# Kernel tuning notes

Measured on AMD Instinct MI355X. Metric: run time of the kernel, lower is better.

## Reference

```python
import jax, jax.numpy as jnp
import numpy as np


def _conv1x1(x, w, b):
    # x: [B,C,H,W], w: [O,C], b: [O] -> [B,O,H,W]
    return jnp.einsum('bchw,oc->bohw', x, w) + b[None, :, None, None]


def _maxpool2x2(x):
    # MaxPool2d(kernel_size=2, stride=2), VALID padding
    return jax.lax.reduce_window(
        x, -jnp.inf, jax.lax.max,
        window_dimensions=(1, 1, 2, 2),
        window_strides=(1, 1, 2, 2),
        padding='VALID')


def setup_inputs() -> dict:
    key = jax.random.key(0)
    ks = jax.random.split(key, 9)
    B, C, H, W = 8, 256, 64, 64
    c = 128  # in_channels // channel_scale_factor
    s = 0.05
    return {
        'x': jax.random.normal(ks[0], (B, C, H, W), jnp.float32),
        'theta_w': jax.random.normal(ks[1], (c, C), jnp.float32) * s,
        'theta_b': jax.random.normal(ks[2], (c,), jnp.float32) * s,
        'phi_w': jax.random.normal(ks[3], (c, C), jnp.float32) * s,
        'phi_b': jax.random.normal(ks[4], (c,), jnp.float32) * s,
        'g_w': jax.random.normal(ks[5], (c, C), jnp.float32) * s,
        'g_b': jax.random.normal(ks[6], (c,), jnp.float32) * s,
        'wz_w': jax.random.normal(ks[7], (C, c), jnp.float32) * s,
        'wz_b': jax.random.normal(ks[8], (C,), jnp.float32) * s,
    }


def reference(x, theta_w, theta_b, phi_w, phi_b, g_w, g_b, wz_w, wz_b):
    B, C, H, W = x.shape
    c = theta_w.shape[0]
    ox = x
    theta = _conv1x1(x, theta_w, theta_b)              # [B,c,H,W]
    xp = _maxpool2x2(x)                                # [B,C,h,w]
    phi = _conv1x1(xp, phi_w, phi_b)                   # [B,c,h,w]
    gi = _conv1x1(xp, g_w, g_b)                        # [B,c,h,w]

    N = H * W
    M = phi.shape[2] * phi.shape[3]
    theta1 = theta.reshape(B, c, N).transpose(0, 2, 1)  # [B,N,c]
    phi1 = phi.reshape(B, c, M)                         # [B,c,M]
    gi1 = gi.reshape(B, c, M).transpose(0, 2, 1)        # [B,M,c]

    m1 = jnp.einsum('bnc,bcm->bnm', theta1, phi1)       # [B,N,M] attention scores
    m1 = jax.nn.softmax(m1, axis=2)
    m2 = jnp.einsum('bnm,bmc->bnc', m1, gi1)            # [B,N,c]
    # Faithful to torch .view: raw-buffer reinterpretation, no transpose
    m3 = m2.reshape(B, c, H, W)
    m4 = _conv1x1(m3, wz_w, wz_b)                       # [B,C,H,W]
    return m4 + ox
```

## Files before the change

### kernel.cpp

```cpp
#include <hip/hip_runtime.h>
#include <math.h>

#define BATCH 8
#define CINCH 256
#define CMID  128
#define NPIX  4096
#define MPIX  1024

typedef __attribute__((ext_vector_type(8))) short bf16x8;
typedef __attribute__((ext_vector_type(4))) short s16x4;
typedef __attribute__((ext_vector_type(4))) float f32x4;

static __device__ __forceinline__ short f2bf(float f) {
    unsigned u = __float_as_uint(f);
    u = (u + 0x7fffu + ((u >> 16) & 1u)) >> 16;
    return (short)u;
}
static __device__ __forceinline__ float bf2f(short s) {
    return __uint_as_float(((unsigned)(unsigned short)s) << 16);
}

static __device__ __forceinline__ void gl16(const void* g, void* l) {
    __builtin_amdgcn_global_load_lds(
        (const __attribute__((address_space(1))) void*)g,
        (__attribute__((address_space(3))) void*)l, 16, 0, 0);
}

__global__ __launch_bounds__(256)
void wcvt_k(const float* __restrict__ a, const float* __restrict__ b,
            const float* __restrict__ c, const float* __restrict__ d,
            short* __restrict__ o)
{
    int i = (blockIdx.x * 256 + threadIdx.x) * 4;
    if (i < 32768) {
        int cr = i >> 8, col = i & 255;
        int R = (cr & 7) * 16 + (cr >> 3);
        float4 v = *(const float4*)(a + i);
        s16x4 rv = { f2bf(v.x * 1.44269504f), f2bf(v.y * 1.44269504f),
                     f2bf(v.z * 1.44269504f), f2bf(v.w * 1.44269504f) };
        *(s16x4*)(o + R * 256 + col) = rv;
    } else {
        const float* src; int j;
        if (i < 65536)      { src = b; j = i - 32768; }
        else if (i < 98304) { src = c; j = i - 65536; }
        else                { src = d; j = i - 98304; }
        float4 v = *(const float4*)(src + j);
        s16x4 rv = { f2bf(v.x), f2bf(v.y), f2bf(v.z), f2bf(v.w) };
        *(s16x4*)(o + i) = rv;
    }
}

__global__ __launch_bounds__(512)
void front_k(const float* __restrict__ x,
             const short* __restrict__ th_wh, const float* __restrict__ th_b,
             const short* __restrict__ ph_wh, const float* __restrict__ ph_b,
             const short* __restrict__ g_wh,  const float* __restrict__ g_b,
             short* __restrict__ thetaO, short* __restrict__ phiO,
             short* __restrict__ gO)
{
    __shared__ float F[128 * 65];
    __shared__ short X[128 * 264];
    __shared__ short P[32 * 264];

    const int bid = blockIdx.x;
    const int t   = threadIdx.x;
    const int b   = bid & 7;
    const int r   = bid >> 3;
    const int wv  = t >> 6;
    const int l   = t & 63;
    const int lr  = l & 15;
    const int lg  = l >> 4;

    const int hh = wv & 1;
    const int c0 = t >> 7;
    float ra[16], rb[16];
    {
        const float* xb = x + ((size_t)(b * 256)) * 4096 + r * 128;
#pragma unroll
        for (int i = 0; i < 16; ++i)
            ra[i] = xb[(size_t)(c0 + i * 4) * 4096 + hh * 64 + l];
    }
#pragma unroll
    for (int ct = 0; ct < 4; ++ct) {
        if ((ct & 1) == 0) {
#pragma unroll
            for (int i = 0; i < 16; ++i) F[(hh * 64 + l) * 65 + c0 + i * 4] = ra[i];
            if (ct < 3) {
                const float* xb = x + ((size_t)(b * 256 + (ct + 1) * 64)) * 4096 + r * 128;
#pragma unroll
                for (int i = 0; i < 16; ++i)
                    rb[i] = xb[(size_t)(c0 + i * 4) * 4096 + hh * 64 + l];
            }
        } else {
#pragma unroll
            for (int i = 0; i < 16; ++i) F[(hh * 64 + l) * 65 + c0 + i * 4] = rb[i];
            if (ct < 3) {
                const float* xb = x + ((size_t)(b * 256 + (ct + 1) * 64)) * 4096 + r * 128;
#pragma unroll
                for (int i = 0; i < 16; ++i)
                    ra[i] = xb[(size_t)(c0 + i * 4) * 4096 + hh * 64 + l];
            }
        }
        asm volatile("s_waitcnt lgkmcnt(0)" ::: "memory");
        __builtin_amdgcn_s_barrier();
#pragma unroll
        for (int i = 0; i < 16; ++i) {
            int row = wv + i * 8;
            X[row * 264 + ct * 64 + l] = f2bf(F[row * 65 + l]);
        }
        asm volatile("s_waitcnt lgkmcnt(0)" ::: "memory");
        __builtin_amdgcn_s_barrier();
    }

#pragma unroll
    for (int i = 0; i < 4; ++i) {
        int slot = i * 512 + t;
        int wp = slot >> 6, c4 = slot & 63;
        s16x4 v0 = *(const s16x4*)(X + (2 * wp) * 264 + c4 * 4);
        s16x4 v1 = *(const s16x4*)(X + (2 * wp + 1) * 264 + c4 * 4);
        s16x4 v2 = *(const s16x4*)(X + (64 + 2 * wp) * 264 + c4 * 4);
        s16x4 v3 = *(const s16x4*)(X + (65 + 2 * wp) * 264 + c4 * 4);
        s16x4 rm;
#pragma unroll
        for (int e = 0; e < 4; ++e) {
            float m = fmaxf(fmaxf(bf2f(v0[e]), bf2f(v1[e])),
                            fmaxf(bf2f(v2[e]), bf2f(v3[e])));
            rm[e] = f2bf(m);
        }
        *(s16x4*)(P + wp * 264 + c4 * 4) = rm;
    }
    __syncthreads();

    {
        const int m0 = wv * 16;
        f32x4 o[8];
#pragma unroll
        for (int dt = 0; dt < 8; ++dt)
#pragma unroll
            for (int e = 0; e < 4; ++e) o[dt][e] = 0.f;
        for (int kt = 0; kt < 8; ++kt) {
            bf16x8 a = *(const bf16x8*)(X + (m0 + lr) * 264 + kt * 32 + lg * 8);
#pragma unroll
            for (int dt = 0; dt < 8; ++dt) {
                bf16x8 bv = *(const bf16x8*)(th_wh + (size_t)(dt * 16 + lr) * 256 + kt * 32 + lg * 8);
                o[dt] = __builtin_amdgcn_mfma_f32_16x16x32_bf16(a, bv, o[dt], 0, 0, 0);
            }
        }
        float bvt[8];
#pragma unroll
        for (int dt = 0; dt < 8; ++dt) bvt[dt] = th_b[lr * 8 + dt] * 1.44269504f;
        short* ob = thetaO + (size_t)b * NPIX * 128;
#pragma unroll
        for (int rr = 0; rr < 4; ++rr) {
            int n = r * 128 + m0 + lg * 4 + rr;
            bf16x8 sv;
#pragma unroll
            for (int dt = 0; dt < 8; ++dt) sv[dt] = f2bf(o[dt][rr] + bvt[dt]);
            *(bf16x8*)(ob + (size_t)n * 128 + lr * 8) = sv;
        }
    }

    {
        const int half = wv & 1;
        const int coH  = (wv >> 1) & 1;
        const short* wsel = ((wv < 4) ? ph_wh : g_wh) + (size_t)coH * 64 * 256;
        const float* bsel = (wv < 4) ? ph_b : g_b;

        f32x4 q[4];
#pragma unroll
        for (int dt = 0; dt < 4; ++dt)
#pragma unroll
            for (int e = 0; e < 4; ++e) q[dt][e] = 0.f;
        for (int kt = 0; kt < 8; ++kt) {
            bf16x8 a = *(const bf16x8*)(P + (half * 16 + lr) * 264 + kt * 32 + lg * 8);
#pragma unroll
            for (int dt = 0; dt < 4; ++dt) {
                bf16x8 bv = *(const bf16x8*)(wsel + (size_t)(dt * 16 + lr) * 256 + kt * 32 + lg * 8);
                q[dt] = __builtin_amdgcn_mfma_f32_16x16x32_bf16(a, bv, q[dt], 0, 0, 0);
            }
        }
        float bv4[4];
#pragma unroll
        for (int dt = 0; dt < 4; ++dt) bv4[dt] = bsel[coH * 64 + dt * 16 + lr];

        if (wv < 4) {
            short* cb = phiO + (size_t)b * 32 * 4096 + (size_t)r * 4096;
#pragma unroll
            for (int rr = 0; rr < 4; ++rr) {
                int mloc = half * 16 + lg * 4 + rr;
                short* cbb = cb + (mloc >> 4) * 512 + (mloc & 15) * 8;
#pragma unroll
                for (int dt = 0; dt < 4; ++dt) {
                    int cc = coH * 64 + dt * 16 + lr;
                    cbb[(cc >> 5) * 1024 + ((cc >> 3) & 3) * 128 + (cc & 7)]
                        = f2bf(q[dt][rr] + bv4[dt]);
                }
            }
        } else {
            short* cb = gO + (size_t)b * 32 * 4096 + (size_t)r * 4096;
            const int keyblk = half * 2 + (lg >> 1);
#pragma unroll
            for (int dt = 0; dt < 4; ++dt) {
                int cc = coH * 64 + dt * 16 + lr;
                s16x4 sv;
#pragma unroll
                for (int rr = 0; rr < 4; ++rr) sv[rr] = f2bf(q[dt][rr] + bv4[dt]);
                *(s16x4*)(cb + (size_t)((cc >> 4) * 64 + keyblk * 16 + (cc & 15)) * 8
                             + (lg & 1) * 4) = sv;
            }
        }
    }
}

__global__ __launch_bounds__(512)
void attn_v10(const short* __restrict__ theta, const short* __restrict__ phi_sw,
              const short* __restrict__ G_sw, short* __restrict__ Z)
{
    __shared__ __align__(16) char smem[147456];
    const int t   = threadIdx.x;
    const int wv  = t >> 6;
    const int l   = t & 63;
    const int lr  = l & 15;
    const int lg  = l >> 4;
    const int gid = wv >> 2;
    const int wvl = wv & 3;
    const int bid = blockIdx.x;
    const int b   = bid & 7;
    const int s   = bid >> 3;

    const short* thb = theta + (size_t)b * NPIX * 128;
    const char*  phC = (const char*)phi_sw + (size_t)b * 32 * 8192;
    const char*  gC  = (const char*)G_sw  + (size_t)b * 32 * 8192;
    const int first = gid * 16;

    auto STAGEP = [&](int bufi, int pi) {
#pragma unroll
        for (int sub = 0; sub < 2; ++sub) {
            int chunk = first + pi * 2 + sub;
            const char* ps = phC + (size_t)chunk * 8192 + wvl * 2048 + l * 16;
            const char* gs = gC  + (size_t)chunk * 8192 + wvl * 2048 + l * 16;
            char* base = smem + gid * 65536 + bufi * 32768 + sub * 16384;
            gl16(ps,        base + wvl * 2048);
            gl16(ps + 1024, base + wvl * 2048 + 1024);
            gl16(gs,        base + 8192 + wvl * 2048);
            gl16(gs + 1024, base + 8192 + wvl * 2048 + 1024);
        }
    };

    STAGEP(0, 0);

    bf16x8 bq[2][4];
#pragma unroll
    for (int u = 0; u < 2; ++u) {
        int n = ((wvl * 2 + u) * 16 + lr) * 32 + s;
#pragma unroll
        for (int kt = 0; kt < 4; ++kt)
            bq[u][kt] = *(const bf16x8*)(thb + (size_t)n * 128 + kt * 32 + lg * 8);
    }

    f32x4 o[2][8];
#pragma unroll
    for (int u = 0; u < 2; ++u)
#pragma unroll
        for (int dt = 0; dt < 8; ++dt)
#pragma unroll
            for (int e = 0; e < 4; ++e) o[u][dt][e] = 0.f;
    float ps_[2] = { 0.f, 0.f };

    for (int pi = 0; pi < 8; ++pi) {
        asm volatile("s_waitcnt vmcnt(0)" ::: "memory");
        __builtin_amdgcn_s_barrier();
        if (pi < 7) STAGEP((pi + 1) & 1, pi + 1);

#pragma unroll
        for (int sub = 0; sub < 2; ++sub) {
            const short* pb = (const short*)(smem + gid * 65536 + (pi & 1) * 32768
                                             + sub * 16384);
            const short* gb = pb + 4096;

            f32x4 ssw[2][2];
#pragma unroll
            for (int u = 0; u < 2; ++u)
#pragma unroll
                for (int mt = 0; mt < 2; ++mt)
#pragma unroll
                    for (int e = 0; e < 4; ++e) ssw[u][mt][e] = 0.f;
#pragma unroll
            for (int kt = 0; kt < 4; ++kt) {
                bf16x8 a0 = *(const bf16x8*)(pb + ((kt * 2 + 0) * 64 + l) * 8);
                bf16x8 a1 = *(const bf16x8*)(pb + ((kt * 2 + 1) * 64 + l) * 8);
#pragma unroll
                for (int u = 0; u < 2; ++u) {
                    ssw[u][0] = __builtin_amdgcn_mfma_f32_16x16x32_bf16(a0, bq[u][kt], ssw[u][0], 0, 0, 0);
                    ssw[u][1] = __builtin_amdgcn_mfma_f32_16x16x32_bf16(a1, bq[u][kt], ssw[u][1], 0, 0, 0);
                }
            }

            bf16x8 gf[8];
#pragma unroll
            for (int dt = 0; dt < 8; ++dt)
                gf[dt] = *(const bf16x8*)(gb + (dt * 64 + l) * 8);

#pragma unroll
            for (int u = 0; u < 2; ++u) {
                short* pu = (short*)(smem + 131072 + wv * 2048 + u * 1024);
#pragma unroll
                for (int mt = 0; mt < 2; ++mt) {
                    s16x4 pv;
#pragma unroll
                    for (int rr = 0; rr < 4; ++rr) {
                        float p = exp2f(ssw[u][mt][rr] - 40.f);
                        ps_[u] += p;
                        pv[rr] = f2bf(p);
                    }
                    *(s16x4*)(pu + ((mt * 2 + (lg >> 1)) * 16 + lr) * 8 + (lg & 1) * 4) = pv;
                }
                bf16x8 pa = *(const bf16x8*)(pu + l * 8);
#pragma unroll
                for (int dt = 0; dt < 8; ++dt)
                    o[u][dt] = __builtin_amdgcn_mfma_f32_16x16x32_bf16(pa, gf[dt], o[u][dt], 0, 0, 0);
            }
        }
    }

    __syncthreads();
    float* mg = (float*)smem;
    if (wv >= 4) {
        float* mb = mg + (size_t)((wv - 4) * 64 + l) * 68;
#pragma unroll
        for (int u = 0; u < 2; ++u)
#pragma unroll
            for (int dt = 0; dt < 8; ++dt)
                *(f32x4*)(mb + (u * 8 + dt) * 4) = o[u][dt];
        mb[64] = ps_[0]; mb[65] = ps_[1];
    }
    __syncthreads();
    if (wv < 4) {
        const float* mb = mg + (size_t)(wv * 64 + l) * 68;
#pragma unroll
        for (int u = 0; u < 2; ++u)
#pragma unroll
            for (int dt = 0; dt < 8; ++dt) {
                f32x4 pv = *(const f32x4*)(mb + (u * 8 + dt) * 4);
#pragma unroll
                for (int e = 0; e < 4; ++e) o[u][dt][e] += pv[e];
            }
        ps_[0] += mb[64]; ps_[1] += mb[65];

        short* Zb = Z + (size_t)b * 16 * 4096 * 8;
#pragma unroll
        for (int u = 0; u < 2; ++u) {
            float tot = ps_[u];
            tot += __shfl_xor(tot, 16);
            tot += __shfl_xor(tot, 32);
            float inv = 1.f / tot;
            float invg[4];
#pragma unroll
            for (int rr = 0; rr < 4; ++rr) invg[rr] = __shfl(inv, lg * 4 + rr);
            const int wq = wvl * 2 + u;
#pragma unroll
            for (int dt = 0; dt < 8; ++dt) {
                s16x4 zv;
#pragma unroll
                for (int rr = 0; rr < 4; ++rr) zv[rr] = f2bf(o[u][dt][rr] * invg[rr]);
                size_t g = (size_t)(wq * 2 + (lg >> 1)) * 4096 + s * 128 + dt * 16 + lr;
                *(s16x4*)(Zb + g * 8 + (lg & 1) * 4) = zv;
            }
        }
    }
}

__global__ __launch_bounds__(256)
void conv_fin_k(const short* __restrict__ Z, const short* __restrict__ wzh,
                const float* __restrict__ wzb, const float* __restrict__ x,
                float* __restrict__ out)
{
    const int t  = threadIdx.x;
    const int wv = t >> 6;
    const int l  = t & 63;
    const int lr = l & 15;
    const int lg = l >> 4;
    const int b  = blockIdx.z;
    const int co0 = blockIdx.y * 64 + (wv >> 1) * 32;
    const int l0  = blockIdx.x * 128 + (wv & 1) * 64;

    bf16x8 afr[2][4];
#pragma unroll
    for (int nt = 0; nt < 2; ++nt) {
        int co = co0 + nt * 16 + lr;
#pragma unroll
        for (int kt = 0; kt < 4; ++kt)
            afr[nt][kt] = *(const bf16x8*)(wzh + (size_t)co * 128 + kt * 32 + lg * 8);
    }

    const short* Zb = Z + (size_t)b * 16 * 4096 * 8;
    f32x4 o[2][4];
#pragma unroll
    for (int nt = 0; nt < 2; ++nt)
#pragma unroll
        for (int dt = 0; dt < 4; ++dt)
#pragma unroll
            for (int e = 0; e < 4; ++e) o[nt][dt][e] = 0.f;

#pragma unroll
    for (int dt = 0; dt < 4; ++dt) {
        int lpix = l0 + dt * 16 + lr;
#pragma unroll
        for (int kt = 0; kt < 4; ++kt) {
            bf16x8 bz = *(const bf16x8*)(Zb + ((size_t)(kt * 4 + lg) * 4096 + lpix) * 8);
            o[0][dt] = __builtin_amdgcn_mfma_f32_16x16x32_bf16(afr[0][kt], bz, o[0][dt], 0, 0, 0);
            o[1][dt] = __builtin_amdgcn_mfma_f32_16x16x32_bf16(afr[1][kt], bz, o[1][dt], 0, 0, 0);
        }
    }

#pragma unroll
    for (int nt = 0; nt < 2; ++nt)
#pragma unroll
        for (int rr = 0; rr < 4; ++rr) {
            int co = co0 + nt * 16 + lg * 4 + rr;
            float bv = wzb[co];
            const float* xb = x + ((size_t)b * 256 + co) * 4096;
            float* ob = out + ((size_t)b * 256 + co) * 4096;
#pragma unroll
            for (int dt = 0; dt < 4; ++dt) {
                int lpix = l0 + dt * 16 + lr;
                ob[lpix] = o[nt][dt][rr] + bv + xb[lpix];
            }
        }
}

extern "C" void kernel_launch(void* const* d_in, const int* in_sizes, int n_in,
                              void* d_out, int out_size, void* d_ws, size_t ws_size,
                              hipStream_t stream)
{
    const float* x       = (const float*)d_in[0];
    const float* theta_w = (const float*)d_in[1];
    const float* theta_b = (const float*)d_in[2];
    const float* phi_w   = (const float*)d_in[3];
    const float* phi_b   = (const float*)d_in[4];
    const float* g_w     = (const float*)d_in[5];
    const float* g_b     = (const float*)d_in[6];
    const float* wz_w    = (const float*)d_in[7];
    const float* wz_b    = (const float*)d_in[8];
    float* out = (float*)d_out;

    short* ws      = (short*)d_ws;
    short* theta_h = ws;
    short* phi_h   = theta_h + (size_t)4194304;
    short* G_h     = phi_h + (size_t)1048576;
    short* Z       = G_h  + (size_t)1048576;
    short* wh      = Z    + (size_t)4194304;
    short* th_wh = wh;
    short* ph_wh = wh + 32768;
    short* g_wh  = wh + 65536;
    short* wz_wh = wh + 98304;

    wcvt_k<<<dim3(128), 256, 0, stream>>>(theta_w, phi_w, g_w, wz_w, wh);

    front_k<<<dim3(256), 512, 0, stream>>>(x, th_wh, theta_b, ph_wh, phi_b,
                                           g_wh, g_b, theta_h, phi_h, G_h);

    attn_v10<<<dim3(256), 512, 0, stream>>>(theta_h, phi_h, G_h, Z);

    conv_fin_k<<<dim3(32, 4, BATCH), 256, 0, stream>>>(Z, wz_wh, wz_b, x, out);
}
```

Before: 89.12 us.

## Fuse output 1x1 conv and residual into attention kernel epilogue

The attention kernel now writes its normalized bf16 output tile into shared memory instead of a global Z buffer. It then runs the wz 1x1 convolution on that tile with MFMA, adding bias and the residual x directly. This removes the separate conv kernel launch and the global round trip of Z. In exchange, each attention block carries extra epilogue work and register pressure, and the weight fragments are loaded per block from global memory.

After: 73.32 us (median of 2 runs). 17.7% less time.

```diff
diff --git a/kernel.cpp b/kernel.cpp
--- a/kernel.cpp
+++ b/kernel.cpp
@@ -213,8 +213,10 @@
 }
 
 __global__ __launch_bounds__(512)
-void attn_v10(const short* __restrict__ theta, const short* __restrict__ phi_sw,
-              const short* __restrict__ G_sw, short* __restrict__ Z)
+void attn_fz(const short* __restrict__ theta, const short* __restrict__ phi_sw,
+             const short* __restrict__ G_sw, const short* __restrict__ wzh,
+             const float* __restrict__ wzb, const float* __restrict__ x,
+             float* __restrict__ out)
 {
     __shared__ __align__(16) char smem[147456];
     const int t   = threadIdx.x;
@@ -325,6 +327,7 @@
 
     __syncthreads();
     float* mg = (float*)smem;
+    short* m3l = (short*)(smem + 73728);
     if (wv >= 4) {
         float* mb = mg + (size_t)((wv - 4) * 64 + l) * 68;
 #pragma unroll
@@ -347,7 +350,6 @@
             }
         ps_[0] += mb[64]; ps_[1] += mb[65];
 
-        short* Zb = Z + (size_t)b * 16 * 4096 * 8;
 #pragma unroll
         for (int u = 0; u < 2; ++u) {
             float tot = ps_[u];
@@ -357,76 +359,61 @@
             float invg[4];
 #pragma unroll
             for (int rr = 0; rr < 4; ++rr) invg[rr] = __shfl(inv, lg * 4 + rr);
-            const int wq = wvl * 2 + u;
+            const int cmb = (wvl * 2 + u) * 2 + (lg >> 1);
 #pragma unroll
             for (int dt = 0; dt < 8; ++dt) {
                 s16x4 zv;
 #pragma unroll
                 for (int rr = 0; rr < 4; ++rr) zv[rr] = f2bf(o[u][dt][rr] * invg[rr]);
-                size_t g = (size_t)(wq * 2 + (lg >> 1)) * 4096 + s * 128 + dt * 16 + lr;
-                *(s16x4*)(Zb + g * 8 + (lg & 1) * 4) = zv;
-            }
-        }
-    }
-}
-
-__global__ __launch_bounds__(256)
-void conv_fin_k(const short* __restrict__ Z, const short* __restrict__ wzh,
-                const float* __restrict__ wzb, const float* __restrict__ x,
-                float* __restrict__ out)
-{
-    const int t  = threadIdx.x;
-    const int wv = t >> 6;
-    const int l  = t & 63;
-    const int lr = l & 15;
-    const int lg = l >> 4;
-    const int b  = blockIdx.z;
-    const int co0 = blockIdx.y * 64 + (wv >> 1) * 32;
-    const int l0  = blockIdx.x * 128 + (wv & 1) * 64;
-
-    bf16x8 afr[2][4];
-#pragma unroll
-    for (int nt = 0; nt < 2; ++nt) {
-        int co = co0 + nt * 16 + lr;
-#pragma unroll
-        for (int kt = 0; kt < 4; ++kt)
-            afr[nt][kt] = *(const bf16x8*)(wzh + (size_t)co * 128 + kt * 32 + lg * 8);
-    }
-
-    const short* Zb = Z + (size_t)b * 16 * 4096 * 8;
-    f32x4 o[2][4];
-#pragma unroll
-    for (int nt = 0; nt < 2; ++nt)
-#pragma unroll
-        for (int dt = 0; dt < 4; ++dt)
-#pragma unroll
-            for (int e = 0; e < 4; ++e) o[nt][dt][e] = 0.f;
-
-#pragma unroll
-    for (int dt = 0; dt < 4; ++dt) {
-        int lpix = l0 + dt * 16 + lr;
-#pragma unroll
-        for (int kt = 0; kt < 4; ++kt) {
-            bf16x8 bz = *(const bf16x8*)(Zb + ((size_t)(kt * 4 + lg) * 4096 + lpix) * 8);
-            o[0][dt] = __builtin_amdgcn_mfma_f32_16x16x32_bf16(afr[0][kt], bz, o[0][dt], 0, 0, 0);
-            o[1][dt] = __builtin_amdgcn_mfma_f32_16x16x32_bf16(afr[1][kt], bz, o[1][dt], 0, 0, 0);
-        }
-    }
-
-#pragma unroll
-    for (int nt = 0; nt < 2; ++nt)
-#pragma unroll
-        for (int rr = 0; rr < 4; ++rr) {
-            int co = co0 + nt * 16 + lg * 4 + rr;
-            float bv = wzb[co];
-            const float* xb = x + ((size_t)b * 256 + co) * 4096;
-            float* ob = out + ((size_t)b * 256 + co) * 4096;
-#pragma unroll
-            for (int dt = 0; dt < 4; ++dt) {
-                int lpix = l0 + dt * 16 + lr;
-                ob[lpix] = o[nt][dt][rr] + bv + xb[lpix];
-            }
-        }
+                *(s16x4*)(m3l + (size_t)(cmb * 128 + dt * 16 + lr) * 8 + (lg & 1) * 4) = zv;
+            }
+        }
+    }
+    __syncthreads();
+
+    {
+        const int co0 = wv * 32;
+        bf16x8 afr[2][4];
+#pragma unroll
+        for (int nt = 0; nt < 2; ++nt) {
+            int co = co0 + nt * 16 + lr;
+#pragma unroll
+            for (int kt = 0; kt < 4; ++kt)
+                afr[nt][kt] = *(const bf16x8*)(wzh + (size_t)co * 128 + kt * 32 + lg * 8);
+        }
+        f32x4 oc[2][8];
+#pragma unroll
+        for (int nt = 0; nt < 2; ++nt)
+#pragma unroll
+            for (int dt = 0; dt < 8; ++dt)
+#pragma unroll
+                for (int e = 0; e < 4; ++e) oc[nt][dt][e] = 0.f;
+
+#pragma unroll
+        for (int dt = 0; dt < 8; ++dt) {
+#pragma unroll
+            for (int kt = 0; kt < 4; ++kt) {
+                bf16x8 bz = *(const bf16x8*)(m3l + (size_t)((kt * 4 + lg) * 128 + dt * 16 + lr) * 8);
+                oc[0][dt] = __builtin_amdgcn_mfma_f32_16x16x32_bf16(afr[0][kt], bz, oc[0][dt], 0, 0, 0);
+                oc[1][dt] = __builtin_amdgcn_mfma_f32_16x16x32_bf16(afr[1][kt], bz, oc[1][dt], 0, 0, 0);
+            }
+        }
+
+#pragma unroll
+        for (int nt = 0; nt < 2; ++nt)
+#pragma unroll
+            for (int rr = 0; rr < 4; ++rr) {
+                int co = co0 + nt * 16 + lg * 4 + rr;
+                float bv = wzb[co];
+                const float* xb = x + ((size_t)b * 256 + co) * 4096 + s * 128;
+                float* ob = out + ((size_t)b * 256 + co) * 4096 + s * 128;
+#pragma unroll
+                for (int dt = 0; dt < 8; ++dt) {
+                    int lp = dt * 16 + lr;
+                    ob[lp] = oc[nt][dt][rr] + bv + xb[lp];
+                }
+            }
+    }
 }
 
 extern "C" void kernel_launch(void* const* d_in, const int* in_sizes, int n_in,
@@ -448,8 +435,7 @@
     short* theta_h = ws;
     short* phi_h   = theta_h + (size_t)4194304;
     short* G_h     = phi_h + (size_t)1048576;
-    short* Z       = G_h  + (size_t)1048576;
-    short* wh      = Z    + (size_t)4194304;
+    short* wh      = G_h  + (size_t)1048576;
     short* th_wh = wh;
     short* ph_wh = wh + 32768;
     short* g_wh  = wh + 65536;
@@ -460,7 +446,6 @@
     front_k<<<dim3(256), 512, 0, stream>>>(x, th_wh, theta_b, ph_wh, phi_b,
                                            g_wh, g_b, theta_h, phi_h, G_h);
 
-    attn_v10<<<dim3(256), 512, 0, stream>>>(theta_h, phi_h, G_h, Z);
-
-    conv_fin_k<<<dim3(32, 4, BATCH), 256, 0, stream>>>(Z, wz_wh, wz_b, x, out);
-}
+    attn_fz<<<dim3(256), 512, 0, stream>>>(theta_h, phi_h, G_h,
+                                           wz_wh, wz_b, x, out);
+}
```
